# Optimization experiments

Hardware: AMD Instinct MI355X
Metric: run time of the kernel (lower is better)

## Reference

```python
import jax, jax.numpy as jnp
import numpy as np

HIDDEN = 2048
INTER = 8192  # shard == INTER since world_size == 1
BATCH, LOCAL_SEQ = 2, 4096


def setup_inputs() -> dict:
    key = jax.random.key(0)
    k1, k2, k3 = jax.random.split(key, 3)
    h_shard = jax.random.normal(k1, (BATCH, LOCAL_SEQ, HIDDEN), dtype=jnp.float32)
    # torch Linear weights are [out_features, in_features]
    w_gate_up = jax.random.normal(k2, (2 * INTER, HIDDEN), dtype=jnp.float32) * 0.02
    w_down = jax.random.normal(k3, (HIDDEN, INTER), dtype=jnp.float32) * 0.02
    return {"h_shard": h_shard, "w_gate_up": w_gate_up, "w_down": w_down}


def reference(h_shard, w_gate_up, w_down):
    # world_size == 1: ag_mm == matmul (all-gather is identity),
    # mm_rs == matmul (reduce-scatter of single partial is identity).
    batch, local_seq, hidden = h_shard.shape
    # gate_up: [b, s, 2*shard]
    gate_up = jnp.einsum('bsh,oh->bso', h_shard, w_gate_up)
    gate, up = jnp.split(gate_up, 2, axis=-1)
    h = jax.nn.silu(gate) * up  # [b, s, shard]
    out = jnp.einsum('bsi,hi->bsh', h, w_down)  # [b, s, hidden]
    return out
```

## Files before the change

kernel.cpp:

```cpp
#include <hip/hip_runtime.h>
#include <hip/hip_bf16.h>
#include <cstdint>
#include <cstddef>

#define HIDDEN 2048
#define INTER 8192
#define M_TOK 8192

typedef __attribute__((ext_vector_type(8))) short short8;
typedef __attribute__((ext_vector_type(4))) float float4v;

typedef __hip_bfloat16 bf16;

__global__ void cvt_bf16(const float* __restrict__ src, bf16* __restrict__ dst, int n) {
    int idx = blockIdx.x * blockDim.x + threadIdx.x;
    int stride = gridDim.x * blockDim.x;
    for (int i = idx * 4; i < n; i += stride * 4) {
        float4 v = *(const float4*)(src + i);
        union { bf16 h[4]; ushort4 u; } pk;
        pk.h[0] = __float2bfloat16(v.x);
        pk.h[1] = __float2bfloat16(v.y);
        pk.h[2] = __float2bfloat16(v.z);
        pk.h[3] = __float2bfloat16(v.w);
        *(ushort4*)(dst + i) = pk.u;
    }
}

__device__ __forceinline__ void load16_lds(const bf16* g, bf16* l) {
    __builtin_amdgcn_global_load_lds((const __attribute__((address_space(1))) void*)g,
                                     (__attribute__((address_space(3))) void*)l,
                                     16, 0, 0);
}

template<int KDIM, bool FUSE>
__global__ __launch_bounds__(512, 2) void gemm_8ph(const bf16* __restrict__ A,
                                                   const bf16* __restrict__ B,
                                                   bf16* __restrict__ actout,
                                                   float* __restrict__ cout) {
    static_assert(KDIM % 64 == 0, "KDIM multiple of 64");
    __shared__ __align__(16) bf16 sm[2 * 32768];

    constexpr int NKT = KDIM / 64;

    const int tid  = threadIdx.x;
    const int wave = tid >> 6;
    const int lane = tid & 63;
    const int wm = wave >> 2;
    const int wn = wave & 3;
    const int lm = lane & 15;
    const int kg = lane >> 4;

    const int id = blockIdx.y * gridDim.x + blockIdx.x;
    const int w_ = id >> 3;
    const int by = (id & 7) * 4 + (w_ & 3);
    const int bx = w_ >> 2;

    const int m0 = by * 256;
    const int n0 = bx * (FUSE ? 128 : 256);

    const int srow = wave * 8 + (lane >> 3);
    const int scol = ((lane & 7) ^ (lane >> 3)) * 8;
    const bf16* ag[4];
    const bf16* bg[4];
#pragma unroll
    for (int q = 0; q < 4; ++q) {
        const int arow = m0 + (q & 1) * 128 + (q >> 1) * 64 + srow;
        ag[q] = A + (size_t)arow * KDIM + scol;
        int brow;
        if (FUSE) {
            brow = n0 + (q >> 1) * (INTER - 128) + q * 64 + srow;
        } else {
            const int t = (q & 1) * 64 + srow;
            brow = n0 + (t >> 5) * 64 + (q >> 1) * 32 + (t & 31);
        }
        bg[q] = B + (size_t)brow * KDIM + scol;
    }
    bf16* const sdA = sm + wave * 512;
    bf16* const sdB = sm + 16384 + wave * 512;

    const int sl0 = ((0 * 4 + kg) ^ (lm & 7)) * 8;
    const int sl1 = ((1 * 4 + kg) ^ (lm & 7)) * 8;

    float4v acc[8][4];
#pragma unroll
    for (int i = 0; i < 8; i++)
#pragma unroll
        for (int j = 0; j < 4; j++) acc[i][j] = (float4v)0.f;

    short8 af[8];
    short8 bq[4];
    short8 bq2[4];

#define STAGE_A(h, nb, kn) { \
        load16_lds(ag[(h)*2+0] + (size_t)(kn)*64, sdA + (nb)*32768 + ((h)*2+0)*4096); \
        load16_lds(ag[(h)*2+1] + (size_t)(kn)*64, sdA + (nb)*32768 + ((h)*2+1)*4096); }
#define STAGE_B(h, nb, kn) { \
        load16_lds(bg[(h)*2+0] + (size_t)(kn)*64, sdB + (nb)*32768 + ((h)*2+0)*4096); \
        load16_lds(bg[(h)*2+1] + (size_t)(kn)*64, sdB + (nb)*32768 + ((h)*2+1)*4096); }
#define LOAD_A(dst, ih, smA_) { \
        _Pragma("unroll") \
        for (int i2 = 0; i2 < 4; i2++) { \
            const bf16* p = (smA_) + ((ih) * 128 + wm * 64 + i2 * 16 + lm) * 64; \
            dst[i2*2+0] = *(const short8*)(p + sl0); \
            dst[i2*2+1] = *(const short8*)(p + sl1); } }
#define LOAD_B(dst, jh, smB_) { \
        _Pragma("unroll") \
        for (int j2 = 0; j2 < 2; j2++) { \
            const bf16* p = (smB_) + ((jh) * 128 + wn * 32 + j2 * 16 + lm) * 64; \
            dst[j2*2+0] = *(const short8*)(p + sl0); \
            dst[j2*2+1] = *(const short8*)(p + sl1); } }
#define MFMA_Q(A_, B_, ih, jh) { \
        _Pragma("unroll") \
        for (int i2 = 0; i2 < 4; i2++) \
        _Pragma("unroll") \
        for (int j2 = 0; j2 < 2; j2++) { \
            acc[(ih)*4+i2][(jh)*2+j2] = __builtin_amdgcn_mfma_f32_16x16x32_bf16(A_[i2*2+0], B_[j2*2+0], acc[(ih)*4+i2][(jh)*2+j2], 0, 0, 0); \
            acc[(ih)*4+i2][(jh)*2+j2] = __builtin_amdgcn_mfma_f32_16x16x32_bf16(A_[i2*2+1], B_[j2*2+1], acc[(ih)*4+i2][(jh)*2+j2], 0, 0, 0); } }
#define FENCE asm volatile("" ::: "memory")
#define BAR   do { FENCE; __builtin_amdgcn_s_barrier(); FENCE; } while (0)
#define VMC4  asm volatile("s_waitcnt vmcnt(4)" ::: "memory")
#define SBAR0 __builtin_amdgcn_sched_barrier(0)

    STAGE_A(0, 0, 0);
    STAGE_B(0, 0, 0);
    STAGE_B(1, 0, 0);
    STAGE_A(1, 0, 0);
    VMC4;
    BAR;
    LOAD_A(af, 0, sm);
    LOAD_B(bq, 0, sm + 16384);

    for (int kt = 0; kt < NKT; ++kt) {
        const int bb = kt & 1;
        const int nb = bb ^ 1;
        const int kn = (kt + 1 < NKT) ? (kt + 1) : 0;
        const bf16* smA  = sm + bb * 32768;
        const bf16* smB  = smA + 16384;
        const bf16* smA2 = sm + nb * 32768;
        const bf16* smB2 = smA2 + 16384;

        STAGE_A(0, nb, kn);
        VMC4;
        BAR;
        __builtin_amdgcn_s_setprio(1);
        MFMA_Q(af, bq, 0, 0);
        __builtin_amdgcn_s_setprio(0);
        SBAR0;
        LOAD_B(bq2, 1, smB);

        STAGE_B(0, nb, kn);
        VMC4;
        BAR;
        __builtin_amdgcn_s_setprio(1);
        MFMA_Q(af, bq2, 0, 1);
        __builtin_amdgcn_s_setprio(0);
        SBAR0;
        LOAD_A(af, 1, smA);

        STAGE_B(1, nb, kn);
        VMC4;
        BAR;
        __builtin_amdgcn_s_setprio(1);
        MFMA_Q(af, bq2, 1, 1);
        __builtin_amdgcn_s_setprio(0);
        SBAR0;

        STAGE_A(1, nb, kn);
        VMC4;
        BAR;
        __builtin_amdgcn_s_setprio(1);
        MFMA_Q(af, bq, 1, 0);
        __builtin_amdgcn_s_setprio(0);
        SBAR0;
        LOAD_A(af, 0, smA2);
        LOAD_B(bq, 0, smB2);
    }
    asm volatile("s_waitcnt vmcnt(0)" ::: "memory");

    if (FUSE) {
        const int orow = m0 + wm * 128;
        const int ocol = n0 + wn * 32;
#pragma unroll
        for (int i = 0; i < 8; i++)
#pragma unroll
            for (int j2 = 0; j2 < 2; j2++)
#pragma unroll
                for (int r = 0; r < 4; r++) {
                    const float g = acc[i][j2][r];
                    const float u = acc[i][j2 + 2][r];
                    const float a = (g / (1.f + __expf(-g))) * u;
                    actout[(size_t)(orow + i * 16 + kg * 4 + r) * INTER + ocol + j2 * 16 + lm] =
                        __float2bfloat16(a);
                }
    } else {
        const int orow = m0 + wm * 128;
        const int ocol = n0 + wn * 64;
#pragma unroll
        for (int i = 0; i < 8; i++)
#pragma unroll
            for (int j = 0; j < 4; j++)
#pragma unroll
                for (int r = 0; r < 4; r++)
                    cout[(size_t)(orow + i * 16 + kg * 4 + r) * HIDDEN + ocol + j * 16 + lm] =
                        acc[i][j][r];
    }
#undef STAGE_A
#undef STAGE_B
#undef LOAD_A
#undef LOAD_B
#undef MFMA_Q
#undef FENCE
#undef BAR
#undef VMC4
#undef SBAR0
}

extern "C" void kernel_launch(void* const* d_in, const int* in_sizes, int n_in,
                              void* d_out, int out_size, void* d_ws, size_t ws_size,
                              hipStream_t stream) {
    const float* h   = (const float*)d_in[0];
    const float* wgu = (const float*)d_in[1];
    const float* wd  = (const float*)d_in[2];
    float* out = (float*)d_out;

    char* ws = (char*)d_ws;
    bf16* hbf   = (bf16*)(ws);
    bf16* wgubf = (bf16*)(ws + 33554432ull);
    bf16* wdbf  = (bf16*)(ws + 100663296ull);
    bf16* actbf = (bf16*)(ws + 134217728ull);

    cvt_bf16<<<dim3(4096), 256, 0, stream>>>(h,   hbf,   M_TOK * HIDDEN);
    cvt_bf16<<<dim3(8192), 256, 0, stream>>>(wgu, wgubf, 2 * INTER * HIDDEN);
    cvt_bf16<<<dim3(4096), 256, 0, stream>>>(wd,  wdbf,  HIDDEN * INTER);

    gemm_8ph<HIDDEN, true><<<dim3(64, 32), 512, 0, stream>>>(hbf, wgubf, actbf, nullptr);

    gemm_8ph<INTER, false><<<dim3(8, 32), 512, 0, stream>>>(actbf, wdbf, nullptr, out);
}
```

Measured before the change: 932.4 us.

## Interleave LDS fragment loads with MFMAs and unroll K loop by two tiles

Restructures the GEMM main loop so the K loop is unrolled by two tiles with ping-pong B register sets. A-fragment reads from LDS are interleaved inside the MFMA groups using sched_group_barrier, and the stage order is reordered. Global pointers are replaced by a single base plus compile-time offsets to save registers. The goal is to hide LDS read latency behind matrix math, at the cost of an extra B register array and stricter KDIM divisibility.

```diff
diff --git a/kernel.cpp b/kernel.cpp
--- a/kernel.cpp
+++ b/kernel.cpp
@@ -37,7 +37,7 @@
                                                    const bf16* __restrict__ B,
                                                    bf16* __restrict__ actout,
                                                    float* __restrict__ cout) {
-    static_assert(KDIM % 64 == 0, "KDIM multiple of 64");
+    static_assert(KDIM % 128 == 0, "KDIM multiple of 128 (tile pairs)");
     __shared__ __align__(16) bf16 sm[2 * 32768];
 
     constexpr int NKT = KDIM / 64;
@@ -60,21 +60,17 @@
 
     const int srow = wave * 8 + (lane >> 3);
     const int scol = ((lane & 7) ^ (lane >> 3)) * 8;
-    const bf16* ag[4];
-    const bf16* bg[4];
-#pragma unroll
-    for (int q = 0; q < 4; ++q) {
-        const int arow = m0 + (q & 1) * 128 + (q >> 1) * 64 + srow;
-        ag[q] = A + (size_t)arow * KDIM + scol;
-        int brow;
-        if (FUSE) {
-            brow = n0 + (q >> 1) * (INTER - 128) + q * 64 + srow;
-        } else {
-            const int t = (q & 1) * 64 + srow;
-            brow = n0 + (t >> 5) * 64 + (q >> 1) * 32 + (t & 31);
-        }
-        bg[q] = B + (size_t)brow * KDIM + scol;
-    }
+
+    const bf16* const aBase = A + (size_t)(m0 + srow) * KDIM + scol;
+    const int brow0 = FUSE ? (n0 + srow)
+                           : (n0 + ((srow >> 5) << 6) + (srow & 31));
+    const bf16* const bBase = B + (size_t)brow0 * KDIM + scol;
+
+#define AOFFQ(q) ((size_t)((((q) & 1) * 128 + ((q) >> 1) * 64)) * KDIM)
+#define BOFFQ(q) (FUSE ? ((size_t)(((q) >> 1) ? (INTER + ((q) & 1) * 64) \
+                                              : (((q) & 1) * 64)) * KDIM) \
+                       : ((size_t)((((q) & 1) * 128 + ((q) >> 1) * 32)) * KDIM))
+
     bf16* const sdA = sm + wave * 512;
     bf16* const sdB = sm + 16384 + wave * 512;
 
@@ -88,15 +84,16 @@
         for (int j = 0; j < 4; j++) acc[i][j] = (float4v)0.f;
 
     short8 af[8];
-    short8 bq[4];
-    short8 bq2[4];
+    short8 b0a[4];
+    short8 b0b[4];
+    short8 b1q[4];
 
 #define STAGE_A(h, nb, kn) { \
-        load16_lds(ag[(h)*2+0] + (size_t)(kn)*64, sdA + (nb)*32768 + ((h)*2+0)*4096); \
-        load16_lds(ag[(h)*2+1] + (size_t)(kn)*64, sdA + (nb)*32768 + ((h)*2+1)*4096); }
+        load16_lds(aBase + AOFFQ((h)*2+0) + (size_t)(kn)*64, sdA + (nb)*32768 + ((h)*2+0)*4096); \
+        load16_lds(aBase + AOFFQ((h)*2+1) + (size_t)(kn)*64, sdA + (nb)*32768 + ((h)*2+1)*4096); }
 #define STAGE_B(h, nb, kn) { \
-        load16_lds(bg[(h)*2+0] + (size_t)(kn)*64, sdB + (nb)*32768 + ((h)*2+0)*4096); \
-        load16_lds(bg[(h)*2+1] + (size_t)(kn)*64, sdB + (nb)*32768 + ((h)*2+1)*4096); }
+        load16_lds(bBase + BOFFQ((h)*2+0) + (size_t)(kn)*64, sdB + (nb)*32768 + ((h)*2+0)*4096); \
+        load16_lds(bBase + BOFFQ((h)*2+1) + (size_t)(kn)*64, sdB + (nb)*32768 + ((h)*2+1)*4096); }
 #define LOAD_A(dst, ih, smA_) { \
         _Pragma("unroll") \
         for (int i2 = 0; i2 < 4; i2++) { \
@@ -116,64 +113,69 @@
         for (int j2 = 0; j2 < 2; j2++) { \
             acc[(ih)*4+i2][(jh)*2+j2] = __builtin_amdgcn_mfma_f32_16x16x32_bf16(A_[i2*2+0], B_[j2*2+0], acc[(ih)*4+i2][(jh)*2+j2], 0, 0, 0); \
             acc[(ih)*4+i2][(jh)*2+j2] = __builtin_amdgcn_mfma_f32_16x16x32_bf16(A_[i2*2+1], B_[j2*2+1], acc[(ih)*4+i2][(jh)*2+j2], 0, 0, 0); } }
+#define MFMA_ILV(A_, B_, ih, jh, rih, smR) { \
+        _Pragma("unroll") \
+        for (int i2 = 0; i2 < 4; i2++) { \
+            acc[(ih)*4+i2][(jh)*2+0] = __builtin_amdgcn_mfma_f32_16x16x32_bf16(A_[i2*2+0], B_[0], acc[(ih)*4+i2][(jh)*2+0], 0, 0, 0); \
+            acc[(ih)*4+i2][(jh)*2+0] = __builtin_amdgcn_mfma_f32_16x16x32_bf16(A_[i2*2+1], B_[1], acc[(ih)*4+i2][(jh)*2+0], 0, 0, 0); \
+            acc[(ih)*4+i2][(jh)*2+1] = __builtin_amdgcn_mfma_f32_16x16x32_bf16(A_[i2*2+0], B_[2], acc[(ih)*4+i2][(jh)*2+1], 0, 0, 0); \
+            acc[(ih)*4+i2][(jh)*2+1] = __builtin_amdgcn_mfma_f32_16x16x32_bf16(A_[i2*2+1], B_[3], acc[(ih)*4+i2][(jh)*2+1], 0, 0, 0); \
+            const bf16* p_ = (smR) + ((rih) * 128 + wm * 64 + i2 * 16 + lm) * 64; \
+            A_[i2*2+0] = *(const short8*)(p_ + sl0); \
+            A_[i2*2+1] = *(const short8*)(p_ + sl1); \
+            __builtin_amdgcn_sched_group_barrier(0x8,   4, 0); \
+            __builtin_amdgcn_sched_group_barrier(0x100, 2, 0); \
+        } }
 #define FENCE asm volatile("" ::: "memory")
 #define BAR   do { FENCE; __builtin_amdgcn_s_barrier(); FENCE; } while (0)
 #define VMC4  asm volatile("s_waitcnt vmcnt(4)" ::: "memory")
 #define SBAR0 __builtin_amdgcn_sched_barrier(0)
 
+#define TILE_BODY(B0C, B0N, BB, KN) { \
+        const bf16* const smCur  = sm + (BB) * 32768; \
+        const bf16* const smCurB = smCur + 16384; \
+        const bf16* const smNxt  = sm + ((BB) ^ 1) * 32768; \
+        const bf16* const smNxtB = smNxt + 16384; \
+         \
+        STAGE_B(0, (BB) ^ 1, KN); \
+        VMC4; BAR; \
+        LOAD_B(b1q, 1, smCurB); \
+        SBAR0; \
+        __builtin_amdgcn_s_setprio(1); MFMA_Q(af, B0C, 0, 0); __builtin_amdgcn_s_setprio(0); \
+        SBAR0; \
+         \
+        STAGE_A(0, (BB) ^ 1, KN); \
+        VMC4; BAR; \
+        __builtin_amdgcn_s_setprio(1); MFMA_ILV(af, b1q, 0, 1, 1, smCur); __builtin_amdgcn_s_setprio(0); \
+        SBAR0; \
+         \
+        STAGE_B(1, (BB) ^ 1, KN); \
+        VMC4; BAR; \
+        LOAD_B(B0N, 0, smNxtB); \
+        SBAR0; \
+        __builtin_amdgcn_s_setprio(1); MFMA_Q(af, b1q, 1, 1); __builtin_amdgcn_s_setprio(0); \
+        SBAR0; \
+         \
+        STAGE_A(1, (BB) ^ 1, KN); \
+        VMC4; BAR; \
+        __builtin_amdgcn_s_setprio(1); MFMA_ILV(af, B0C, 1, 0, 0, smNxt); __builtin_amdgcn_s_setprio(0); \
+        SBAR0; \
+    }
+
+    STAGE_B(0, 0, 0);
     STAGE_A(0, 0, 0);
-    STAGE_B(0, 0, 0);
     STAGE_B(1, 0, 0);
     STAGE_A(1, 0, 0);
     VMC4;
     BAR;
     LOAD_A(af, 0, sm);
-    LOAD_B(bq, 0, sm + 16384);
-
-    for (int kt = 0; kt < NKT; ++kt) {
-        const int bb = kt & 1;
-        const int nb = bb ^ 1;
-        const int kn = (kt + 1 < NKT) ? (kt + 1) : 0;
-        const bf16* smA  = sm + bb * 32768;
-        const bf16* smB  = smA + 16384;
-        const bf16* smA2 = sm + nb * 32768;
-        const bf16* smB2 = smA2 + 16384;
-
-        STAGE_A(0, nb, kn);
-        VMC4;
-        BAR;
-        __builtin_amdgcn_s_setprio(1);
-        MFMA_Q(af, bq, 0, 0);
-        __builtin_amdgcn_s_setprio(0);
-        SBAR0;
-        LOAD_B(bq2, 1, smB);
-
-        STAGE_B(0, nb, kn);
-        VMC4;
-        BAR;
-        __builtin_amdgcn_s_setprio(1);
-        MFMA_Q(af, bq2, 0, 1);
-        __builtin_amdgcn_s_setprio(0);
-        SBAR0;
-        LOAD_A(af, 1, smA);
-
-        STAGE_B(1, nb, kn);
-        VMC4;
-        BAR;
-        __builtin_amdgcn_s_setprio(1);
-        MFMA_Q(af, bq2, 1, 1);
-        __builtin_amdgcn_s_setprio(0);
-        SBAR0;
-
-        STAGE_A(1, nb, kn);
-        VMC4;
-        BAR;
-        __builtin_amdgcn_s_setprio(1);
-        MFMA_Q(af, bq, 1, 0);
-        __builtin_amdgcn_s_setprio(0);
-        SBAR0;
-        LOAD_A(af, 0, smA2);
-        LOAD_B(bq, 0, smB2);
+    LOAD_B(b0a, 0, sm + 16384);
+
+    for (int kt = 0; kt < NKT; kt += 2) {
+        const int kn1 = kt + 1;
+        TILE_BODY(b0a, b0b, 0, kn1);
+        const int kn2 = (kt + 2 < NKT) ? (kt + 2) : 0;
+        TILE_BODY(b0b, b0a, 1, kn2);
     }
     asm volatile("s_waitcnt vmcnt(0)" ::: "memory");
 
@@ -209,10 +211,14 @@
 #undef LOAD_A
 #undef LOAD_B
 #undef MFMA_Q
+#undef MFMA_ILV
 #undef FENCE
 #undef BAR
 #undef VMC4
 #undef SBAR0
+#undef TILE_BODY
+#undef AOFFQ
+#undef BOFFQ
 }
 
 extern "C" void kernel_launch(void* const* d_in, const int* in_sizes, int n_in,
```

After: 941.9 us. Within noise of the previous version (+1.0%).
